# Kernel tuning notes

Hardware: AMD Instinct MI355X
Metric: run time of the kernel (lower is better)

## Reference

```python
import jax, jax.numpy as jnp
import numpy as np

OUT_FEATURES = 4096
IN_FEATURES = 16384
NNZ = 2_000_000
BATCH = 128


def setup_inputs() -> dict:
    key = jax.random.key(0)
    k1, k2, k3, k4, k5 = jax.random.split(key, 5)
    inputs = jax.random.normal(k1, (BATCH, IN_FEATURES), dtype=jnp.float32)
    # learned sparse weight values and bias (uniform init like reset_parameters)
    bound = 1.0 / (IN_FEATURES ** 0.5)
    values = jax.random.uniform(k2, (NNZ,), minval=-bound, maxval=bound, dtype=jnp.float32)
    bias = jax.random.uniform(k3, (OUT_FEATURES,), minval=-bound, maxval=bound, dtype=jnp.float32)
    # fixed COO connectivity: rows -> out_features, cols -> in_features
    rows = jax.random.randint(k4, (NNZ,), 0, OUT_FEATURES, dtype=jnp.int32)
    cols = jax.random.randint(k5, (NNZ,), 0, IN_FEATURES, dtype=jnp.int32)
    return {"inputs": inputs, "values": values, "bias": bias, "rows": rows, "cols": cols}


def reference(inputs, values, bias, rows, cols):
    # out[b, r] = sum_{k: rows[k]==r} values[k] * inputs[b, cols[k]]  (+ bias[r])
    # Gather input columns per nnz entry, scale, then scatter-add into output rows.
    contrib = inputs[:, cols] * values            # [B, nnz]
    out = jax.ops.segment_sum(contrib.T, rows, num_segments=OUT_FEATURES).T  # [B, out_features]
    return out + bias
```

## Files before the change

### kernel.cpp

```cpp
#include <hip/hip_runtime.h>
#include <hip/hip_fp16.h>

#define NNZ    2000000
#define BATCH  128
#define IN_F   16384
#define OUT_F  4096
#define NCH    512
#define CHUNK  3912
#define NBK    1024
#define RPB    4
#define BK_CAP 2240

__device__ inline int mbcnt64(unsigned long long m) {
  return __builtin_amdgcn_mbcnt_hi((unsigned)(m >> 32),
         __builtin_amdgcn_mbcnt_lo((unsigned)m, 0));
}


__global__ __launch_bounds__(512)
void k_localsort(const int* __restrict__ rows, const int* __restrict__ cols,
                 const float* __restrict__ vals, int* __restrict__ desc,
                 unsigned* __restrict__ pairs) {
  __shared__ unsigned stage[CHUNK];
  __shared__ int h[NBK], cur[NBK];
  __shared__ int wsums[8];
  const int t = threadIdx.x, c = blockIdx.x;
  const int lane = t & 63, w = t >> 6;
  const int base = c * CHUNK;
  const int n = min(CHUNK, NNZ - base);
  const int n4 = n >> 2;

  h[t] = 0; h[t + 512] = 0;
  __syncthreads();
  for (int i = t; i < n4; i += 512) {
    const int4 r4 = ((const int4*)(rows + base))[i];
    atomicAdd(&h[r4.x >> 2], 1);
    atomicAdd(&h[r4.y >> 2], 1);
    atomicAdd(&h[r4.z >> 2], 1);
    atomicAdd(&h[r4.w >> 2], 1);
  }
  __syncthreads();
  const int v0 = h[2 * t], v1 = h[2 * t + 1];
  const int sv = v0 + v1;
  int x = sv;
#pragma unroll
  for (int off = 1; off < 64; off <<= 1) { int y = __shfl_up(x, off); if (lane >= off) x += y; }
  if (lane == 63) wsums[w] = x;
  __syncthreads();
  int wex = 0;
#pragma unroll
  for (int j = 0; j < 8; ++j) { const int sj = wsums[j]; wex += (j < w) ? sj : 0; }
  const int excl = wex + x - sv;
  cur[2 * t] = excl;
  cur[2 * t + 1] = excl + v0;
  ((int2*)desc)[c * 512 + t] = make_int2((excl << 8) | v0, ((excl + v0) << 8) | v1);
  __syncthreads();
  for (int i = t; i < n4; i += 512) {
    const int4   r4 = ((const int4*)(rows + base))[i];
    const int4   c4 = ((const int4*)(cols + base))[i];
    const float4 f4 = ((const float4*)(vals + base))[i];
    int pos;
    pos = atomicAdd(&cur[r4.x >> 2], 1);
    stage[pos] = ((unsigned)c4.x << 18) | ((unsigned)(r4.x & 3) << 16) | (unsigned)__half_as_ushort(__float2half(f4.x));
    pos = atomicAdd(&cur[r4.y >> 2], 1);
    stage[pos] = ((unsigned)c4.y << 18) | ((unsigned)(r4.y & 3) << 16) | (unsigned)__half_as_ushort(__float2half(f4.y));
    pos = atomicAdd(&cur[r4.z >> 2], 1);
    stage[pos] = ((unsigned)c4.z << 18) | ((unsigned)(r4.z & 3) << 16) | (unsigned)__half_as_ushort(__float2half(f4.z));
    pos = atomicAdd(&cur[r4.w >> 2], 1);
    stage[pos] = ((unsigned)c4.w << 18) | ((unsigned)(r4.w & 3) << 16) | (unsigned)__half_as_ushort(__float2half(f4.w));
  }
  __syncthreads();
  for (int j = t; j < n4; j += 512)
    ((uint4*)(pairs + base))[j] = ((const uint4*)stage)[j];
}

__global__ __launch_bounds__(256)
void k_dtr(const int* __restrict__ desc, int* __restrict__ descT) {
  __shared__ int tile[32][33];
  const int tx = threadIdx.x, ty = threadIdx.y;
  const int x0 = blockIdx.x * 32, y0 = blockIdx.y * 32;
#pragma unroll
  for (int j = 0; j < 32; j += 8)
    tile[ty + j][tx] = desc[(y0 + ty + j) * NBK + x0 + tx];
  __syncthreads();
#pragma unroll
  for (int j = 0; j < 32; j += 8)
    descT[(x0 + ty + j) * NCH + y0 + tx] = tile[tx][ty + j];
}

__global__ __launch_bounds__(256)
void k_cscan(const int* __restrict__ descT, unsigned* __restrict__ rdesc,
             int* __restrict__ btot) {
  const int t = threadIdx.x, lane = t & 63, w = t >> 6;
  const int b = blockIdx.x * 4 + w;
  int carry = 0;
#pragma unroll
  for (int j = 0; j < 8; ++j) {
    const int cc = j * 64 + lane;
    const unsigned d = (unsigned)descT[b * NCH + cc];
    const int len = (int)(d & 255u);
    int x = len;
#pragma unroll
    for (int off = 1; off < 64; off <<= 1) { int y = __shfl_up(x, off); if (lane >= off) x += y; }
    rdesc[b * NCH + cc] = (d << 12) | (unsigned)(carry + x - len);
    carry += __shfl(x, 63);
  }
  if (lane == 0) btot[b] = carry;
}

__global__ __launch_bounds__(256)
void k_transpose(const float* __restrict__ in, __half* __restrict__ inT) {
  __shared__ float tile[32][33];
  const int tx = threadIdx.x, ty = threadIdx.y;
  const int c0 = blockIdx.x * 32, b0 = blockIdx.y * 32;
#pragma unroll
  for (int j = 0; j < 32; j += 8)
    tile[ty + j][tx] = in[(b0 + ty + j) * IN_F + c0 + tx];
  __syncthreads();
#pragma unroll
  for (int j = 0; j < 32; j += 8)
    inT[(size_t)(c0 + ty + j) * BATCH + b0 + tx] = __float2half(tile[tx][ty + j]);
}

#define REFILL(SL, KK) do { \
    const int idx = (hh_ + 2 * (KK)) * 8 + 2 * g; \
    const bool vld = idx < nr; \
    const int i0_ = vld ? (s + idx) : 0; \
    uint2 pp = *((const uint2*)(sorted + i0_)); \
    if (!vld) { pp.x &= 0xffff0000u; pp.y &= 0xffff0000u; } \
    x##SL##0 = inT[(pp.x >> 18) * 16 + q]; \
    x##SL##1 = inT[(pp.y >> 18) * 16 + q]; \
    pv##SL = pp; \
  } while (0)

#define FMAH(SL) do { \
    const __half2 hv0 = __half2half2(__ushort_as_half((unsigned short)(pv##SL.x & 0xffffu))); \
    const __half2 hv1 = __half2half2(__ushort_as_half((unsigned short)(pv##SL.y & 0xffffu))); \
    const __half2* h0 = (const __half2*)&x##SL##0; \
    const __half2* h1 = (const __half2*)&x##SL##1; \
    hac0 = __hfma2(hv0, h0[0], hac0); hac1 = __hfma2(hv0, h0[1], hac1); \
    hac2 = __hfma2(hv0, h0[2], hac2); hac3 = __hfma2(hv0, h0[3], hac3); \
    hac0 = __hfma2(hv1, h1[0], hac0); hac1 = __hfma2(hv1, h1[1], hac1); \
    hac2 = __hfma2(hv1, h1[2], hac2); hac3 = __hfma2(hv1, h1[3], hac3); \
  } while (0)

#define STAGE(SL, NEXTKK) do { FMAH(SL); REFILL(SL, NEXTKK); } while (0)

#define FLUSH() do { \
    float2 f0 = __half22float2(hac0), f1 = __half22float2(hac1); \
    float2 f2 = __half22float2(hac2), f3 = __half22float2(hac3); \
    a0 += f0.x; a1 += f0.y; a2 += f1.x; a3 += f1.y; \
    a4 += f2.x; a5 += f2.y; a6 += f3.x; a7 += f3.y; \
    hac0 = hz; hac1 = hz; hac2 = hz; hac3 = hz; \
  } while (0)

__global__ __launch_bounds__(512, 8)
void k_spmm(const uint4* __restrict__ inT, const unsigned* __restrict__ pairs,
            const unsigned* __restrict__ rdesc, const int* __restrict__ btot,
            const float* __restrict__ bias, float* __restrict__ out) {
  __shared__ __align__(16) unsigned staging[BK_CAP];
  __shared__ __align__(16) unsigned sorted[BK_CAP + 8];
  __shared__ int  exd[NCH];
  __shared__ int  wrun[32];
  __shared__ unsigned long long wmask[32];
  __shared__ int  wcnt[32];
  __shared__ int  lst[RPB + 1];
  const int t = threadIdx.x, b = blockIdx.x;
  const int w = t >> 6, lane = t & 63;
  const int n = min(btot[b], BK_CAP);
  const int nrnd = (n + 511) & ~511;

  if (t < NCH) exd[t] = (int)rdesc[b * NCH + t];
  __syncthreads();
  for (int i = t; i < n; i += 512) {
    int lo = 0, hi = NCH - 1;
#pragma unroll
    for (int st = 0; st < 9; ++st) {
      const int mid = (lo + hi + 1) >> 1;
      if ((exd[mid] & 4095) <= i) lo = mid; else hi = mid - 1;
    }
    const unsigned d = (unsigned)exd[lo];
    staging[i] = pairs[lo * CHUNK + (int)(d >> 20) + (i - (int)(d & 4095u))];
  }
  __syncthreads();

  int cnt = 0;
  for (int i = w * 64 + lane; i < nrnd; i += 512) {
    const bool valid = i < n;
    const unsigned key = valid ? staging[i] : 0u;
    const int r4 = valid ? (int)((key >> 16) & 3u) : 4;
    unsigned long long m[4];
#pragma unroll
    for (int r = 0; r < 4; ++r) m[r] = __ballot(r4 == r);
    if (lane < 4) cnt += __popcll(m[lane]);
  }
  if (lane < 4) wcnt[w * 4 + lane] = cnt;
  __syncthreads();

  if (w == 0 && lane < 32) {
    const int v = wcnt[lane];
    int x = v;
#pragma unroll
    for (int off = 4; off < 32; off <<= 1) { int y = __shfl_up(x, off); if (lane >= off) x += y; }
    const int exw = x - v;
    int lstr = 0, tpad = 0;
#pragma unroll
    for (int rr = 0; rr < 4; ++rr) {
      const int tr = __shfl(x, 28 + rr);
      const int trE = (tr + 1) & ~1;
      if ((lane & 3) > rr) lstr += trE;
      tpad += trE;
    }
    wrun[lane] = lstr + exw;
    if (lane < 4) lst[lane] = lstr;
    if (lane == 0) lst[RPB] = tpad;
    if (lane >= 28) {
      if (x & 1) sorted[lstr + x] = 0u;
    }
  }
  __syncthreads();

  for (int i = w * 64 + lane; i < nrnd; i += 512) {
    const bool valid = i < n;
    const unsigned p = valid ? staging[i] : 0u;
    const int r4 = valid ? (int)((p >> 16) & 3u) : 4;
    unsigned long long m[4];
#pragma unroll
    for (int r = 0; r < 4; ++r) m[r] = __ballot(r4 == r);
    if (lane < 4) wmask[w * 4 + lane] = m[lane];
    if (valid) {
      const int rank = wrun[w * 4 + r4] + mbcnt64(wmask[w * 4 + r4]);
      sorted[rank] = p;
    }
    if (lane < 4) wrun[w * 4 + lane] += __popcll(m[lane]);
  }
  __syncthreads();

  const int rloc = w >> 1, hh_ = w & 1;
  const int r = b * RPB + rloc;
  const int g = lane >> 4, q = lane & 15;
  const int s = lst[rloc];
  const int nr = lst[rloc + 1] - s;
  const int nsteps = (nr + 7) >> 3;
  const int K = (nsteps + 1) >> 1;
  const int K3 = ((K + 2) / 3) * 3;

  float a0 = 0.f, a1 = 0.f, a2 = 0.f, a3 = 0.f, a4 = 0.f, a5 = 0.f, a6 = 0.f, a7 = 0.f;
  const __half2 hz = __float2half2_rn(0.f);
  __half2 hac0 = hz, hac1 = hz, hac2 = hz, hac3 = hz;
  uint4 xA0, xA1, xB0, xB1, xC0, xC1;
  uint2 pvA, pvB, pvC;

  REFILL(A, 0);
  REFILL(B, 1);
  REFILL(C, 2);
  for (int kk = 0; kk < K3; kk += 3) {
    STAGE(A, kk + 3);
    STAGE(B, kk + 4);
    STAGE(C, kk + 5);
    FLUSH();
  }

  a0 += __shfl_xor(a0, 16); a0 += __shfl_xor(a0, 32);
  a1 += __shfl_xor(a1, 16); a1 += __shfl_xor(a1, 32);
  a2 += __shfl_xor(a2, 16); a2 += __shfl_xor(a2, 32);
  a3 += __shfl_xor(a3, 16); a3 += __shfl_xor(a3, 32);
  a4 += __shfl_xor(a4, 16); a4 += __shfl_xor(a4, 32);
  a5 += __shfl_xor(a5, 16); a5 += __shfl_xor(a5, 32);
  a6 += __shfl_xor(a6, 16); a6 += __shfl_xor(a6, 32);
  a7 += __shfl_xor(a7, 16); a7 += __shfl_xor(a7, 32);

  float (*part)[BATCH] = (float (*)[BATCH])staging;
  if (hh_ == 1 && g == 0) {
    const int o = q * 8;
    part[rloc][o + 0] = a0; part[rloc][o + 1] = a1;
    part[rloc][o + 2] = a2; part[rloc][o + 3] = a3;
    part[rloc][o + 4] = a4; part[rloc][o + 5] = a5;
    part[rloc][o + 6] = a6; part[rloc][o + 7] = a7;
  }
  __syncthreads();
  if (hh_ == 0 && g == 0) {
    const float bs_ = bias[r];
    const int o = q * 8;
    out[(o + 0) * OUT_F + r] = a0 + part[rloc][o + 0] + bs_;
    out[(o + 1) * OUT_F + r] = a1 + part[rloc][o + 1] + bs_;
    out[(o + 2) * OUT_F + r] = a2 + part[rloc][o + 2] + bs_;
    out[(o + 3) * OUT_F + r] = a3 + part[rloc][o + 3] + bs_;
    out[(o + 4) * OUT_F + r] = a4 + part[rloc][o + 4] + bs_;
    out[(o + 5) * OUT_F + r] = a5 + part[rloc][o + 5] + bs_;
    out[(o + 6) * OUT_F + r] = a6 + part[rloc][o + 6] + bs_;
    out[(o + 7) * OUT_F + r] = a7 + part[rloc][o + 7] + bs_;
  }
}

extern "C" void kernel_launch(void* const* d_in, const int* in_sizes, int n_in,
                              void* d_out, int out_size, void* d_ws, size_t ws_size,
                              hipStream_t stream) {
  const float* inputs = (const float*)d_in[0];
  const float* values = (const float*)d_in[1];
  const float* bias   = (const float*)d_in[2];
  const int*   rows   = (const int*)d_in[3];
  const int*   cols   = (const int*)d_in[4];
  float* out = (float*)d_out;

  char* ws = (char*)d_ws;
  __half*   inputT = (__half*)(ws);
  unsigned* pairs  = (unsigned*)(ws + 4194304);
  int*      desc   = (int*)(ws + 12206080);
  int*      descT  = (int*)(ws + 14303232);
  unsigned* rdesc  = (unsigned*)descT;
  int*      btot   = (int*)(ws + 16400384);

  k_localsort<<<NCH,     512, 0, stream>>>(rows, cols, values, desc, pairs);
  k_dtr      <<<dim3(NBK / 32, NCH / 32), dim3(32, 8), 0, stream>>>(desc, descT);
  k_cscan    <<<NBK / 4, 256, 0, stream>>>(descT, rdesc, btot);
  k_transpose<<<dim3(IN_F / 32, BATCH / 32), dim3(32, 8), 0, stream>>>(inputs, inputT);
  k_spmm     <<<NBK,     512, 0, stream>>>((const uint4*)inputT, pairs, rdesc, btot, bias, out);
}
```

Measured before the change: 123.3 us.

## Fuse descriptor transpose, column scan and input transpose into one kernel

Merges the descriptor transpose, per-bucket scan and input fp32-to-fp16 transpose into a single launch. Block ranges are split by role: the first 128 blocks each transpose 8 bucket columns in shared memory and scan them directly, and the remaining blocks transpose 64-column input tiles using vectorized float4 loads and uint4 stores. The local sort also caches the row indices in shared memory so the second pass does not reread them from global memory. The goal is to remove two launches, the intermediate descT round trip and the redundant global row reads, at the cost of extra shared memory and a heterogeneous grid.

Result: no change. 122.3 us (-0.8%).

```diff
diff --git a/kernel.cpp b/kernel.cpp
--- a/kernel.cpp
+++ b/kernel.cpp
@@ -22,6 +22,7 @@
                  const float* __restrict__ vals, int* __restrict__ desc,
                  unsigned* __restrict__ pairs) {
   __shared__ unsigned stage[CHUNK];
+  __shared__ int lrows[CHUNK];
   __shared__ int h[NBK], cur[NBK];
   __shared__ int wsums[8];
   const int t = threadIdx.x, c = blockIdx.x;
@@ -34,6 +35,7 @@
   __syncthreads();
   for (int i = t; i < n4; i += 512) {
     const int4 r4 = ((const int4*)(rows + base))[i];
+    ((int4*)lrows)[i] = r4;
     atomicAdd(&h[r4.x >> 2], 1);
     atomicAdd(&h[r4.y >> 2], 1);
     atomicAdd(&h[r4.z >> 2], 1);
@@ -56,7 +58,7 @@
   ((int2*)desc)[c * 512 + t] = make_int2((excl << 8) | v0, ((excl + v0) << 8) | v1);
   __syncthreads();
   for (int i = t; i < n4; i += 512) {
-    const int4   r4 = ((const int4*)(rows + base))[i];
+    const int4   r4 = ((const int4*)lrows)[i];
     const int4   c4 = ((const int4*)(cols + base))[i];
     const float4 f4 = ((const float4*)(vals + base))[i];
     int pos;
@@ -75,51 +77,67 @@
 }
 
 __global__ __launch_bounds__(256)
-void k_dtr(const int* __restrict__ desc, int* __restrict__ descT) {
-  __shared__ int tile[32][33];
-  const int tx = threadIdx.x, ty = threadIdx.y;
-  const int x0 = blockIdx.x * 32, y0 = blockIdx.y * 32;
-#pragma unroll
-  for (int j = 0; j < 32; j += 8)
-    tile[ty + j][tx] = desc[(y0 + ty + j) * NBK + x0 + tx];
-  __syncthreads();
-#pragma unroll
-  for (int j = 0; j < 32; j += 8)
-    descT[(x0 + ty + j) * NCH + y0 + tx] = tile[tx][ty + j];
-}
-
-__global__ __launch_bounds__(256)
-void k_cscan(const int* __restrict__ descT, unsigned* __restrict__ rdesc,
-             int* __restrict__ btot) {
+void k_mid(const int* __restrict__ desc, unsigned* __restrict__ rdesc,
+           int* __restrict__ btot, const float* __restrict__ in,
+           __half* __restrict__ inT) {
+  __shared__ __align__(16) char smem[33280];
   const int t = threadIdx.x, lane = t & 63, w = t >> 6;
-  const int b = blockIdx.x * 4 + w;
-  int carry = 0;
-#pragma unroll
-  for (int j = 0; j < 8; ++j) {
-    const int cc = j * 64 + lane;
-    const unsigned d = (unsigned)descT[b * NCH + cc];
-    const int len = (int)(d & 255u);
-    int x = len;
-#pragma unroll
-    for (int off = 1; off < 64; off <<= 1) { int y = __shfl_up(x, off); if (lane >= off) x += y; }
-    rdesc[b * NCH + cc] = (d << 12) | (unsigned)(carry + x - len);
-    carry += __shfl(x, 63);
-  }
-  if (lane == 0) btot[b] = carry;
-}
-
-__global__ __launch_bounds__(256)
-void k_transpose(const float* __restrict__ in, __half* __restrict__ inT) {
-  __shared__ float tile[32][33];
-  const int tx = threadIdx.x, ty = threadIdx.y;
-  const int c0 = blockIdx.x * 32, b0 = blockIdx.y * 32;
-#pragma unroll
-  for (int j = 0; j < 32; j += 8)
-    tile[ty + j][tx] = in[(b0 + ty + j) * IN_F + c0 + tx];
-  __syncthreads();
-#pragma unroll
-  for (int j = 0; j < 32; j += 8)
-    inT[(size_t)(c0 + ty + j) * BATCH + b0 + tx] = __float2half(tile[tx][ty + j]);
+
+  if (blockIdx.x < 128) {
+    int (*tl)[520] = (int (*)[520])smem;
+    const int b0 = blockIdx.x * 8;
+#pragma unroll
+    for (int p = 0; p < 16; ++p) {
+      const int idx = p * 256 + t;
+      const int cc = idx >> 3, j = idx & 7;
+      tl[j][cc] = desc[cc * NBK + b0 + j];
+    }
+    __syncthreads();
+#pragma unroll
+    for (int jj = 0; jj < 2; ++jj) {
+      const int j = w + jj * 4;
+      int carry = 0;
+#pragma unroll
+      for (int p = 0; p < 8; ++p) {
+        const int cc = p * 64 + lane;
+        const unsigned d = (unsigned)tl[j][cc];
+        const int len = (int)(d & 255u);
+        int x = len;
+#pragma unroll
+        for (int off = 1; off < 64; off <<= 1) { int y = __shfl_up(x, off); if (lane >= off) x += y; }
+        rdesc[(b0 + j) * NCH + cc] = (d << 12) | (unsigned)(carry + x - len);
+        carry += __shfl(x, 63);
+      }
+      if (lane == 0) btot[b0 + j] = carry;
+    }
+  } else {
+    float* tileF = (float*)smem;
+    const int c0 = (blockIdx.x - 128) * 64;
+    const int q4 = t & 15, bq = t >> 4;
+#pragma unroll
+    for (int p = 0; p < 8; ++p) {
+      const int b = p * 16 + bq;
+      const float4 v = *(const float4*)(in + (size_t)b * IN_F + c0 + q4 * 4);
+      float* dst = tileF + b * 65 + q4 * 4;
+      dst[0] = v.x; dst[1] = v.y; dst[2] = v.z; dst[3] = v.w;
+    }
+    __syncthreads();
+    const int oct = t & 15, cl0 = t >> 4;
+#pragma unroll
+    for (int p = 0; p < 4; ++p) {
+      const int cl = p * 16 + cl0;
+      const float* src = tileF + oct * 8 * 65 + cl;
+      unsigned u0 = (unsigned)__half_as_ushort(__float2half(src[0]))
+                  | ((unsigned)__half_as_ushort(__float2half(src[65])) << 16);
+      unsigned u1 = (unsigned)__half_as_ushort(__float2half(src[130]))
+                  | ((unsigned)__half_as_ushort(__float2half(src[195])) << 16);
+      unsigned u2 = (unsigned)__half_as_ushort(__float2half(src[260]))
+                  | ((unsigned)__half_as_ushort(__float2half(src[325])) << 16);
+      unsigned u3 = (unsigned)__half_as_ushort(__float2half(src[390]))
+                  | ((unsigned)__half_as_ushort(__float2half(src[455])) << 16);
+      ((uint4*)inT)[(size_t)(c0 + cl) * 16 + oct] = make_uint4(u0, u1, u2, u3);
+    }
+  }
 }
 
 #define REFILL(SL, KK) do { \
@@ -307,13 +325,10 @@
   __half*   inputT = (__half*)(ws);
   unsigned* pairs  = (unsigned*)(ws + 4194304);
   int*      desc   = (int*)(ws + 12206080);
-  int*      descT  = (int*)(ws + 14303232);
-  unsigned* rdesc  = (unsigned*)descT;
+  unsigned* rdesc  = (unsigned*)(ws + 14303232);
   int*      btot   = (int*)(ws + 16400384);
 
-  k_localsort<<<NCH,     512, 0, stream>>>(rows, cols, values, desc, pairs);
-  k_dtr      <<<dim3(NBK / 32, NCH / 32), dim3(32, 8), 0, stream>>>(desc, descT);
-  k_cscan    <<<NBK / 4, 256, 0, stream>>>(descT, rdesc, btot);
-  k_transpose<<<dim3(IN_F / 32, BATCH / 32), dim3(32, 8), 0, stream>>>(inputs, inputT);
-  k_spmm     <<<NBK,     512, 0, stream>>>((const uint4*)inputT, pairs, rdesc, btot, bias, out);
-}
+  k_localsort<<<NCH, 512, 0, stream>>>(rows, cols, values, desc, pairs);
+  k_mid      <<<384, 256, 0, stream>>>(desc, rdesc, btot, inputs, inputT);
+  k_spmm     <<<NBK, 512, 0, stream>>>((const uint4*)inputT, pairs, rdesc, btot, bias, out);
+}
```
